# Optimization experiments

Hardware: AMD Instinct MI355X
Metric: run time of the kernel (lower is better)

## Reference

```python
import jax, jax.numpy as jnp
import numpy as np

WS = 7          # window size (7x7)
N = WS * WS     # tokens per window = 49
C = 192         # channels
H = 6           # heads
NW = 64         # windows per image (for mask)
B_ = 8192       # num_windows * batch


def _rel_index():
    coords = np.stack(np.meshgrid(np.arange(WS), np.arange(WS), indexing='ij'))  # [2,7,7]
    cf = coords.reshape(2, -1)                       # [2,49]
    rc = (cf[:, :, None] - cf[:, None, :]).transpose(1, 2, 0).astype(np.int64)  # [49,49,2]
    rc[..., 0] += WS - 1
    rc[..., 1] += WS - 1
    rc[..., 0] *= 2 * WS - 1
    return jnp.asarray(rc.sum(-1), dtype=jnp.int32)  # [49,49], values in [0, 169)


def setup_inputs() -> dict:
    key = jax.random.key(0)
    ks = jax.random.split(key, 10)
    std = 0.02
    return {
        'xq': jax.random.normal(ks[0], (B_, N, C), dtype=jnp.float32),
        'mask': jax.random.normal(ks[1], (NW, N, N), dtype=jnp.float32),
        'Wq': jax.random.normal(ks[2], (C, C), dtype=jnp.float32) * std,
        'bq': jnp.zeros((C,), dtype=jnp.float32),
        'Wkv': jax.random.normal(ks[3], (C, 2 * C), dtype=jnp.float32) * std,
        'bkv': jnp.zeros((2 * C,), dtype=jnp.float32),
        'Wproj': jax.random.normal(ks[4], (C, C), dtype=jnp.float32) * std,
        'bproj': jnp.zeros((C,), dtype=jnp.float32),
        'bias_table': jax.random.normal(ks[5], ((2 * WS - 1) * (2 * WS - 1), H), dtype=jnp.float32) * std,
        'rel_index': _rel_index(),
    }


def reference(xq, mask, Wq, bq, Wkv, bkv, Wproj, bproj, bias_table, rel_index):
    b_, n, c = xq.shape
    h = H
    dh = c // h
    scale = dh ** (-0.5)
    # projections (xkv = xq since xkv is None in the original call)
    q = (xq @ Wq + bq).reshape(b_, n, h, dh).transpose(0, 2, 1, 3) * scale      # [b_,h,n,dh]
    kv = (xq @ Wkv + bkv).reshape(b_, n, 2, h, dh).transpose(2, 0, 3, 1, 4)     # [2,b_,h,n,dh]
    k, v = kv[0], kv[1]
    attn = jnp.einsum('bhqd,bhkd->bhqk', q, k)                                   # [b_,h,n,n]
    # gathered relative-position bias: [n,n,h] -> [h,n,n]
    bias = bias_table[rel_index.reshape(-1)].reshape(n, n, h).transpose(2, 0, 1)
    attn = attn + bias[None]
    # mask add: [b_//nw, nw, h, n, n] + [1, nw, 1, n, n]
    nw = mask.shape[0]
    attn = attn.reshape(b_ // nw, nw, h, n, n) + mask[None, :, None]
    attn = jax.nn.softmax(attn.reshape(b_, h, n, n), axis=-1)
    x = jnp.einsum('bhqk,bhkd->bhqd', attn, v).transpose(0, 2, 1, 3).reshape(b_, n, c)
    return x @ Wproj + bproj
```

## Files before the change

kernel.cpp:

```cpp
#include <hip/hip_runtime.h>


#define NTOK 49
#define NPAD 64
#define CCH 192
#define NHEAD 6
#define DH 32

typedef __bf16 bf16_t;
typedef bf16_t bf16x8 __attribute__((ext_vector_type(8)));
typedef bf16_t bf16x4 __attribute__((ext_vector_type(4)));
typedef float f32x4 __attribute__((ext_vector_type(4)));

#define WS_WQT   0
#define WS_WKVT  73728
#define WS_WPT   221184
#define WS_BIASG 294912

__global__ void prep_kernel(const float* __restrict__ Wq, const float* __restrict__ Wkv,
                            const float* __restrict__ Wproj, const float* __restrict__ btab,
                            const int* __restrict__ rel,
                            bf16_t* __restrict__ wqt, bf16_t* __restrict__ wkvt,
                            bf16_t* __restrict__ wpt, float* __restrict__ biasg) {
    int i = blockIdx.x * 256 + threadIdx.x;
    if (i < 36864) { int n = i / 192, k = i % 192; wqt[i] = (bf16_t)Wq[k * 192 + n]; }
    int j = i - 36864;
    if (j >= 0 && j < 73728) { int n = j / 192, k = j % 192; wkvt[j] = (bf16_t)Wkv[k * 384 + n]; }
    int p = i - 110592;
    if (p >= 0 && p < 36864) { int n = p / 192, k = p % 192; wpt[p] = (bf16_t)Wproj[k * 192 + n]; }
    int q = i - 147456;
    if (q >= 0 && q < 14406) { int h = q / 2401, rc = q % 2401; biasg[q] = btab[rel[rc] * 6 + h]; }
}

__global__ __launch_bounds__(512) void wattn_kernel(
    const float* __restrict__ xq, const float* __restrict__ mask,
    const float* __restrict__ bq, const float* __restrict__ bkv, const float* __restrict__ bproj,
    const bf16_t* __restrict__ wqt, const bf16_t* __restrict__ wkvt, const bf16_t* __restrict__ wpt,
    const float* __restrict__ biasg, float* __restrict__ out)
{
    __shared__ __align__(16) unsigned char smem[114688];
    unsigned char* Xs = smem;
    unsigned char* Qs = smem + 24576;
    unsigned char* Ks = smem + 49152;
    unsigned char* Vt = smem + 73728;
    unsigned char* Ps = smem + 98304;

    const int tid = threadIdx.x;
    const int wid = tid >> 6;
    const int lane = tid & 63;
    const int l15 = lane & 15;
    const int lg = lane >> 4;
    const int b = blockIdx.x;
    const float* xp = xq + (size_t)b * (NTOK * CCH);

    for (int idx = tid; idx < 2352; idx += 512) {
        int row = idx / 48;
        int cb = (idx % 48) * 4;
        float4 v = *(const float4*)(xp + row * 192 + cb);
        bf16x4 pk = { (bf16_t)v.x, (bf16_t)v.y, (bf16_t)v.z, (bf16_t)v.w };
        *(bf16x4*)(Xs + row * 384 + ((cb * 2) ^ ((row & 7) << 4))) = pk;
    }
    for (int idx = tid; idx < 720; idx += 512) {
        *(unsigned long long*)(Xs + 49 * 384 + idx * 8) = 0ULL;
    }
    __syncthreads();

    const float SCALE = 0.17677669529663687f;
    for (int nt = wid; nt < 36; nt += 8) {
        int m = nt / 12;
        int ncol = (nt % 12) * 16;
        const bf16_t* WT; const float* bias;
        if (m == 0)      { WT = wqt  + (size_t)ncol * 192;        bias = bq + ncol; }
        else if (m == 1) { WT = wkvt + (size_t)ncol * 192;        bias = bkv + ncol; }
        else             { WT = wkvt + (size_t)(192 + ncol) * 192; bias = bkv + 192 + ncol; }
        bf16x8 bfr[6];
        const bf16_t* wrow = WT + (size_t)l15 * 192 + lg * 8;
#pragma unroll
        for (int ks = 0; ks < 6; ks++) bfr[ks] = *(const bf16x8*)(wrow + ks * 32);
        float bv = bias[l15];
#pragma unroll
        for (int mt = 0; mt < 4; mt++) {
            f32x4 acc = { bv, bv, bv, bv };
#pragma unroll
            for (int ks = 0; ks < 6; ks++) {
                int row = mt * 16 + l15;
                int cb = ks * 32 + lg * 8;
                bf16x8 a = *(const bf16x8*)(Xs + row * 384 + ((cb * 2) ^ ((row & 7) << 4)));
                acc = __builtin_amdgcn_mfma_f32_16x16x32_bf16(a, bfr[ks], acc, 0, 0, 0);
            }
            if (m == 0) {
#pragma unroll
                for (int j = 0; j < 4; j++) acc[j] *= SCALE;
            }
#pragma unroll
            for (int j = 0; j < 4; j++) {
                int col = ncol + l15;
                if (m == 2) {
                    int rr = col;
                    int tc = mt * 16 + lg * 4 + j;
                    *(bf16_t*)(Vt + rr * 128 + ((tc * 2) ^ ((rr & 7) << 4))) = (bf16_t)acc[j];
                } else {
                    int rr = mt * 16 + lg * 4 + j;
                    unsigned char* dst = (m == 0) ? Qs : Ks;
                    *(bf16_t*)(dst + rr * 384 + ((col * 2) ^ ((rr & 7) << 4))) = (bf16_t)acc[j];
                }
            }
        }
    }
    __syncthreads();

    const int widx = b & 63;
    const float* maskw = mask + (size_t)widx * 2401;
    unsigned char* Pw = Ps + wid * 2048;

    for (int k3 = 0; k3 < 3; k3++) {
        int u = wid + 8 * k3;
        int h = u >> 2, qt = u & 3;
        int qrow = qt * 16 + l15;
        int qcb = h * 32 + lg * 8;
        bf16x8 afr = *(const bf16x8*)(Qs + qrow * 384 + ((qcb * 2) ^ ((qrow & 7) << 4)));
        f32x4 s[4];
#pragma unroll
        for (int f = 0; f < 4; f++) {
            int krow = f * 16 + l15;
            bf16x8 kfr = *(const bf16x8*)(Ks + krow * 384 + ((qcb * 2) ^ ((krow & 7) << 4)));
            f32x4 z = { 0.f, 0.f, 0.f, 0.f };
            s[f] = __builtin_amdgcn_mfma_f32_16x16x32_bf16(afr, kfr, z, 0, 0, 0);
        }
        const float* bgh = biasg + h * 2401;
#pragma unroll
        for (int f = 0; f < 4; f++) {
            int c = f * 16 + l15;
#pragma unroll
            for (int j = 0; j < 4; j++) {
                int r = qt * 16 + lg * 4 + j;
                if (c >= 49) s[f][j] = -1e30f;
                else if (r < 49) s[f][j] += bgh[r * 49 + c] + maskw[r * 49 + c];
            }
        }
        float mx[4], rs[4];
#pragma unroll
        for (int j = 0; j < 4; j++) {
            float m0 = fmaxf(fmaxf(s[0][j], s[1][j]), fmaxf(s[2][j], s[3][j]));
#pragma unroll
            for (int d = 1; d < 16; d <<= 1) m0 = fmaxf(m0, __shfl_xor(m0, d, 16));
            mx[j] = m0;
        }
#pragma unroll
        for (int j = 0; j < 4; j++) {
            float t = 0.f;
#pragma unroll
            for (int f = 0; f < 4; f++) { s[f][j] = __expf(s[f][j] - mx[j]); t += s[f][j]; }
#pragma unroll
            for (int d = 1; d < 16; d <<= 1) t += __shfl_xor(t, d, 16);
            rs[j] = 1.0f / t;
        }
#pragma unroll
        for (int f = 0; f < 4; f++) {
            int c = f * 16 + l15;
#pragma unroll
            for (int j = 0; j < 4; j++) {
                int rr = lg * 4 + j;
                *(bf16_t*)(Pw + rr * 128 + ((c * 2) ^ ((rr & 7) << 4))) = (bf16_t)(s[f][j] * rs[j]);
            }
        }
        __threadfence_block();
        bf16x8 pa[2];
#pragma unroll
        for (int ks = 0; ks < 2; ks++) {
            int pcb = ks * 32 + lg * 8;
            pa[ks] = *(const bf16x8*)(Pw + l15 * 128 + ((pcb * 2) ^ ((l15 & 7) << 4)));
        }
#pragma unroll
        for (int dt = 0; dt < 2; dt++) {
            f32x4 acc = { 0.f, 0.f, 0.f, 0.f };
#pragma unroll
            for (int ks = 0; ks < 2; ks++) {
                int vr = h * 32 + dt * 16 + l15;
                int vcb = ks * 32 + lg * 8;
                bf16x8 vfr = *(const bf16x8*)(Vt + vr * 128 + ((vcb * 2) ^ ((vr & 7) << 4)));
                acc = __builtin_amdgcn_mfma_f32_16x16x32_bf16(pa[ks], vfr, acc, 0, 0, 0);
            }
#pragma unroll
            for (int j = 0; j < 4; j++) {
                int orow = qt * 16 + lg * 4 + j;
                int ocol = h * 32 + dt * 16 + l15;
                *(bf16_t*)(Xs + orow * 384 + ((ocol * 2) ^ ((orow & 7) << 4))) = (bf16_t)acc[j];
            }
        }
    }
    __syncthreads();

    float* op = out + (size_t)b * (NTOK * CCH);
    for (int nt = wid; nt < 12; nt += 8) {
        int ncol = nt * 16;
        bf16x8 bfr[6];
        const bf16_t* wrow = wpt + (size_t)(ncol + l15) * 192 + lg * 8;
#pragma unroll
        for (int ks = 0; ks < 6; ks++) bfr[ks] = *(const bf16x8*)(wrow + ks * 32);
        float bv = bproj[ncol + l15];
#pragma unroll
        for (int mt = 0; mt < 4; mt++) {
            f32x4 acc = { bv, bv, bv, bv };
#pragma unroll
            for (int ks = 0; ks < 6; ks++) {
                int row = mt * 16 + l15;
                int cb = ks * 32 + lg * 8;
                bf16x8 a = *(const bf16x8*)(Xs + row * 384 + ((cb * 2) ^ ((row & 7) << 4)));
                acc = __builtin_amdgcn_mfma_f32_16x16x32_bf16(a, bfr[ks], acc, 0, 0, 0);
            }
#pragma unroll
            for (int j = 0; j < 4; j++) {
                int r = mt * 16 + lg * 4 + j;
                if (r < 49) op[r * 192 + ncol + l15] = acc[j];
            }
        }
    }
}

extern "C" void kernel_launch(void* const* d_in, const int* in_sizes, int n_in,
                              void* d_out, int out_size, void* d_ws, size_t ws_size,
                              hipStream_t stream) {
    const float* xq    = (const float*)d_in[0];
    const float* mask  = (const float*)d_in[1];
    const float* Wq    = (const float*)d_in[2];
    const float* bq    = (const float*)d_in[3];
    const float* Wkv   = (const float*)d_in[4];
    const float* bkv   = (const float*)d_in[5];
    const float* Wproj = (const float*)d_in[6];
    const float* bproj = (const float*)d_in[7];
    const float* btab  = (const float*)d_in[8];
    const int*   rel   = (const int*)d_in[9];
    float* out = (float*)d_out;

    char* ws = (char*)d_ws;
    bf16_t* wqt   = (bf16_t*)(ws + WS_WQT);
    bf16_t* wkvt  = (bf16_t*)(ws + WS_WKVT);
    bf16_t* wpt   = (bf16_t*)(ws + WS_WPT);
    float*  biasg = (float*)(ws + WS_BIASG);

    prep_kernel<<<633, 256, 0, stream>>>(Wq, Wkv, Wproj, btab, rel, wqt, wkvt, wpt, biasg);
    wattn_kernel<<<8192, 512, 0, stream>>>(xq, mask, bq, bkv, bproj, wqt, wkvt, wpt, biasg, out);
}
```

Baseline: 733.7 us.

## Double block to 1024 threads, precombine bias+mask table, vectorize MFMA stores

Launches 16 waves per window instead of 8 and rebalances the QKV, attention and output-projection work evenly across them. The attention scale is folded into Wq and bq in the prep kernel, and relative bias plus mask is precombined into a padded table so each lane reads float4 values. Operand order of the MFMAs is swapped so results come out transposed, which allows packed bf16x4 and float4 stores and a two-shuffle softmax reduction. The costs are a larger prep kernel that writes about 4MB, a larger LDS footprint, and higher register pressure at 1024 threads.

```diff
diff --git a/kernel.cpp b/kernel.cpp
--- a/kernel.cpp
+++ b/kernel.cpp
@@ -2,10 +2,7 @@
 
 
 #define NTOK 49
-#define NPAD 64
 #define CCH 192
-#define NHEAD 6
-#define DH 32
 
 typedef __bf16 bf16_t;
 typedef bf16_t bf16x8 __attribute__((ext_vector_type(8)));
@@ -15,35 +12,57 @@
 #define WS_WQT   0
 #define WS_WKVT  73728
 #define WS_WPT   221184
-#define WS_BIASG 294912
-
-__global__ void prep_kernel(const float* __restrict__ Wq, const float* __restrict__ Wkv,
-                            const float* __restrict__ Wproj, const float* __restrict__ btab,
-                            const int* __restrict__ rel,
+#define WS_BQS   294912
+#define WS_TBL   295680
+
+#define SWZ(row, off) ((off) ^ (((row) & 7) << 4))
+
+__global__ void prep_kernel(const float* __restrict__ Wq, const float* __restrict__ bq,
+                            const float* __restrict__ Wkv, const float* __restrict__ Wproj,
+                            const float* __restrict__ btab, const int* __restrict__ rel,
+                            const float* __restrict__ mask,
                             bf16_t* __restrict__ wqt, bf16_t* __restrict__ wkvt,
-                            bf16_t* __restrict__ wpt, float* __restrict__ biasg) {
-    int i = blockIdx.x * 256 + threadIdx.x;
-    if (i < 36864) { int n = i / 192, k = i % 192; wqt[i] = (bf16_t)Wq[k * 192 + n]; }
-    int j = i - 36864;
-    if (j >= 0 && j < 73728) { int n = j / 192, k = j % 192; wkvt[j] = (bf16_t)Wkv[k * 384 + n]; }
-    int p = i - 110592;
-    if (p >= 0 && p < 36864) { int n = p / 192, k = p % 192; wpt[p] = (bf16_t)Wproj[k * 192 + n]; }
-    int q = i - 147456;
-    if (q >= 0 && q < 14406) { int h = q / 2401, rc = q % 2401; biasg[q] = btab[rel[rc] * 6 + h]; }
+                            bf16_t* __restrict__ wpt, float* __restrict__ bqs,
+                            float* __restrict__ tbl, int mode) {
+    const float SC = 0.17677669529663687f;
+    long i = (long)blockIdx.x * 256 + threadIdx.x;
+    if (i < 36864) { int n = i / 192, k = i % 192; wqt[i] = (bf16_t)(Wq[k * 192 + n] * SC); return; }
+    i -= 36864;
+    if (i < 73728) { int n = i / 192, k = i % 192; wkvt[i] = (bf16_t)Wkv[k * 384 + n]; return; }
+    i -= 73728;
+    if (i < 36864) { int n = i / 192, k = i % 192; wpt[i] = (bf16_t)Wproj[k * 192 + n]; return; }
+    i -= 36864;
+    if (i < 192) { bqs[i] = bq[i] * SC; return; }
+    i -= 192;
+    if (mode == 0) {
+        if (i < 979072) {
+            int c = i % 52; long r = i / 52; int q = r % 49; r /= 49; int h = r % 6; int w = r / 6;
+            tbl[i] = (c < 49) ? (btab[rel[q * 49 + c] * 6 + h] + mask[(size_t)w * 2401 + q * 49 + c]) : 0.f;
+        }
+    } else if (mode == 1) {
+        if (i < 15288) { int c = i % 52; int r = i / 52; int q = r % 49; int h = r / 49;
+            tbl[i] = (c < 49) ? btab[rel[q * 49 + c] * 6 + h] : 0.f; return; }
+        i -= 15288;
+        if (i < 163072) { int c = i % 52; long r = i / 52; int q = r % 49; int w = r / 49;
+            tbl[15288 + i] = (c < 49) ? mask[(size_t)w * 2401 + q * 49 + c] : 0.f; }
+    } else {
+        if (i < 14406) { int h = i / 2401, rc = i % 2401; tbl[i] = btab[rel[rc] * 6 + h]; }
+    }
 }
 
-__global__ __launch_bounds__(512) void wattn_kernel(
+__global__ __launch_bounds__(1024, 4) void wattn_kernel(
     const float* __restrict__ xq, const float* __restrict__ mask,
-    const float* __restrict__ bq, const float* __restrict__ bkv, const float* __restrict__ bproj,
+    const float* __restrict__ bkv, const float* __restrict__ bproj,
     const bf16_t* __restrict__ wqt, const bf16_t* __restrict__ wkvt, const bf16_t* __restrict__ wpt,
-    const float* __restrict__ biasg, float* __restrict__ out)
+    const float* __restrict__ bqs, const float* __restrict__ tbl,
+    float* __restrict__ out, int mode)
 {
-    __shared__ __align__(16) unsigned char smem[114688];
-    unsigned char* Xs = smem;
-    unsigned char* Qs = smem + 24576;
-    unsigned char* Ks = smem + 49152;
-    unsigned char* Vt = smem + 73728;
-    unsigned char* Ps = smem + 98304;
+    __shared__ __align__(16) unsigned char smem[131072];
+    unsigned char* XsO = smem;
+    unsigned char* Qs  = smem + 24576;
+    unsigned char* Ks  = smem + 49152;
+    unsigned char* Vt  = smem + 73728;
+    unsigned char* Ps  = smem + 98304;
 
     const int tid = threadIdx.x;
     const int wid = tid >> 6;
@@ -53,166 +72,176 @@
     const int b = blockIdx.x;
     const float* xp = xq + (size_t)b * (NTOK * CCH);
 
-    for (int idx = tid; idx < 2352; idx += 512) {
+    for (int idx = tid; idx < 2352; idx += 1024) {
         int row = idx / 48;
-        int cb = (idx % 48) * 4;
-        float4 v = *(const float4*)(xp + row * 192 + cb);
+        int c4 = idx % 48;
+        float4 v = *(const float4*)(xp + row * 192 + c4 * 4);
         bf16x4 pk = { (bf16_t)v.x, (bf16_t)v.y, (bf16_t)v.z, (bf16_t)v.w };
-        *(bf16x4*)(Xs + row * 384 + ((cb * 2) ^ ((row & 7) << 4))) = pk;
-    }
-    for (int idx = tid; idx < 720; idx += 512) {
-        *(unsigned long long*)(Xs + 49 * 384 + idx * 8) = 0ULL;
-    }
+        *(bf16x4*)(XsO + row * 384 + SWZ(row, c4 * 8)) = pk;
+    }
+    if (tid < 720) *(unsigned long long*)(XsO + 49 * 384 + tid * 8) = 0ULL;
     __syncthreads();
 
-    const float SCALE = 0.17677669529663687f;
-    for (int nt = wid; nt < 36; nt += 8) {
-        int m = nt / 12;
-        int ncol = (nt % 12) * 16;
-        const bf16_t* WT; const float* bias;
-        if (m == 0)      { WT = wqt  + (size_t)ncol * 192;        bias = bq + ncol; }
-        else if (m == 1) { WT = wkvt + (size_t)ncol * 192;        bias = bkv + ncol; }
-        else             { WT = wkvt + (size_t)(192 + ncol) * 192; bias = bkv + 192 + ncol; }
+    {
         bf16x8 bfr[6];
-        const bf16_t* wrow = WT + (size_t)l15 * 192 + lg * 8;
-#pragma unroll
-        for (int ks = 0; ks < 6; ks++) bfr[ks] = *(const bf16x8*)(wrow + ks * 32);
-        float bv = bias[l15];
-#pragma unroll
-        for (int mt = 0; mt < 4; mt++) {
-            f32x4 acc = { bv, bv, bv, bv };
-#pragma unroll
-            for (int ks = 0; ks < 6; ks++) {
-                int row = mt * 16 + l15;
-                int cb = ks * 32 + lg * 8;
-                bf16x8 a = *(const bf16x8*)(Xs + row * 384 + ((cb * 2) ^ ((row & 7) << 4)));
-                acc = __builtin_amdgcn_mfma_f32_16x16x32_bf16(a, bfr[ks], acc, 0, 0, 0);
-            }
-            if (m == 0) {
-#pragma unroll
-                for (int j = 0; j < 4; j++) acc[j] *= SCALE;
+        float4 bias4;
+        float bv = 0.f;
+        int prev_ut = -1;
+        for (int u = 9 * wid; u < 9 * wid + 9; ++u) {
+            int ut = u >> 2, mt = u & 3;
+            bool isV = (ut >= 24);
+            if (ut != prev_ut) {
+                prev_ut = ut;
+                const bf16_t* wrow;
+                if (ut < 12)      wrow = wqt  + (size_t)(ut * 16 + l15) * 192;
+                else if (ut < 24) wrow = wkvt + (size_t)((ut - 12) * 16 + l15) * 192;
+                else              wrow = wkvt + (size_t)(192 + (ut - 24) * 16 + l15) * 192;
+#pragma unroll
+                for (int ks = 0; ks < 6; ks++) bfr[ks] = *(const bf16x8*)(wrow + ks * 32 + lg * 8);
+                if (!isV) {
+                    const float* bp = (ut < 12) ? (bqs + ut * 16) : (bkv + (ut - 12) * 16);
+                    bias4 = *(const float4*)(bp + lg * 4);
+                } else {
+                    bv = bkv[192 + (ut - 24) * 16 + l15];
+                }
+            }
+            int xrow = mt * 16 + l15;
+            bf16x8 xf[6];
+#pragma unroll
+            for (int ks = 0; ks < 6; ks++)
+                xf[ks] = *(const bf16x8*)(XsO + xrow * 384 + SWZ(xrow, ks * 64 + lg * 16));
+            if (!isV) {
+                f32x4 acc = { bias4.x, bias4.y, bias4.z, bias4.w };
+#pragma unroll
+                for (int ks = 0; ks < 6; ks++)
+                    acc = __builtin_amdgcn_mfma_f32_16x16x32_bf16(bfr[ks], xf[ks], acc, 0, 0, 0);
+                int ncol = (ut < 12 ? ut : ut - 12) * 16;
+                unsigned char* dst = (ut < 12) ? Qs : Ks;
+                bf16x4 pk = { (bf16_t)acc[0], (bf16_t)acc[1], (bf16_t)acc[2], (bf16_t)acc[3] };
+                int trow = mt * 16 + l15;
+                *(bf16x4*)(dst + trow * 384 + SWZ(trow, ncol * 2 + lg * 8)) = pk;
+            } else {
+                f32x4 acc = { bv, bv, bv, bv };
+#pragma unroll
+                for (int ks = 0; ks < 6; ks++)
+                    acc = __builtin_amdgcn_mfma_f32_16x16x32_bf16(xf[ks], bfr[ks], acc, 0, 0, 0);
+                int crow = (ut - 24) * 16 + l15;
+                bf16x4 pk = { (bf16_t)acc[0], (bf16_t)acc[1], (bf16_t)acc[2], (bf16_t)acc[3] };
+                *(bf16x4*)(Vt + crow * 128 + SWZ(crow, mt * 32 + lg * 8)) = pk;
+            }
+        }
+    }
+    __syncthreads();
+
+    const int widx = b & 63;
+    unsigned char* Pw = Ps + wid * 2048;
+    for (int u = wid; u < 24; u += 16) {
+        int h = u >> 2, qt = u & 3;
+        int cb = h * 64 + lg * 16;
+        int qrow = qt * 16 + l15;
+        bf16x8 qfr = *(const bf16x8*)(Qs + qrow * 384 + SWZ(qrow, cb));
+        f32x4 s[4];
+#pragma unroll
+        for (int f = 0; f < 4; f++) {
+            int kr = f * 16 + l15;
+            bf16x8 kfr = *(const bf16x8*)(Ks + kr * 384 + SWZ(kr, cb));
+            f32x4 z = { 0.f, 0.f, 0.f, 0.f };
+            s[f] = __builtin_amdgcn_mfma_f32_16x16x32_bf16(kfr, qfr, z, 0, 0, 0);
+        }
+        int q = qt * 16 + l15;
+        bool qok = (q < 49);
+#pragma unroll
+        for (int f = 0; f < 4; f++) {
+            int kb = f * 16 + lg * 4;
+            float4 a = { 0.f, 0.f, 0.f, 0.f };
+            if (qok && kb < 49) {
+                if (mode == 0) {
+                    a = *(const float4*)(tbl + (((size_t)(widx * 6 + h) * 49 + q) * 52 + kb));
+                } else if (mode == 1) {
+                    float4 b1 = *(const float4*)(tbl + ((size_t)(h * 49 + q) * 52 + kb));
+                    float4 m1 = *(const float4*)(tbl + 15288 + (((size_t)widx * 49 + q) * 52 + kb));
+                    a.x = b1.x + m1.x; a.y = b1.y + m1.y; a.z = b1.z + m1.z; a.w = b1.w + m1.w;
+                }
             }
 #pragma unroll
             for (int j = 0; j < 4; j++) {
-                int col = ncol + l15;
-                if (m == 2) {
-                    int rr = col;
-                    int tc = mt * 16 + lg * 4 + j;
-                    *(bf16_t*)(Vt + rr * 128 + ((tc * 2) ^ ((rr & 7) << 4))) = (bf16_t)acc[j];
-                } else {
-                    int rr = mt * 16 + lg * 4 + j;
-                    unsigned char* dst = (m == 0) ? Qs : Ks;
-                    *(bf16_t*)(dst + rr * 384 + ((col * 2) ^ ((rr & 7) << 4))) = (bf16_t)acc[j];
+                int k = kb + j;
+                float av = (j == 0) ? a.x : (j == 1) ? a.y : (j == 2) ? a.z : a.w;
+                if (mode == 2) {
+                    av = 0.f;
+                    if (qok && k < 49)
+                        av = tbl[h * 2401 + q * 49 + k] + mask[(size_t)widx * 2401 + q * 49 + k];
                 }
-            }
-        }
-    }
-    __syncthreads();
-
-    const int widx = b & 63;
-    const float* maskw = mask + (size_t)widx * 2401;
-    unsigned char* Pw = Ps + wid * 2048;
-
-    for (int k3 = 0; k3 < 3; k3++) {
-        int u = wid + 8 * k3;
-        int h = u >> 2, qt = u & 3;
-        int qrow = qt * 16 + l15;
-        int qcb = h * 32 + lg * 8;
-        bf16x8 afr = *(const bf16x8*)(Qs + qrow * 384 + ((qcb * 2) ^ ((qrow & 7) << 4)));
-        f32x4 s[4];
+                if (k >= 49) s[f][j] = -1e30f;
+                else if (qok) s[f][j] += av;
+            }
+        }
+        float m = -1e30f;
+#pragma unroll
+        for (int f = 0; f < 4; f++)
+#pragma unroll
+            for (int j = 0; j < 4; j++) m = fmaxf(m, s[f][j]);
+        m = fmaxf(m, __shfl_xor(m, 16));
+        m = fmaxf(m, __shfl_xor(m, 32));
+        float t = 0.f;
+#pragma unroll
+        for (int f = 0; f < 4; f++)
+#pragma unroll
+            for (int j = 0; j < 4; j++) { s[f][j] = __expf(s[f][j] - m); t += s[f][j]; }
+        t += __shfl_xor(t, 16);
+        t += __shfl_xor(t, 32);
+        float inv = 1.0f / t;
 #pragma unroll
         for (int f = 0; f < 4; f++) {
-            int krow = f * 16 + l15;
-            bf16x8 kfr = *(const bf16x8*)(Ks + krow * 384 + ((qcb * 2) ^ ((krow & 7) << 4)));
-            f32x4 z = { 0.f, 0.f, 0.f, 0.f };
-            s[f] = __builtin_amdgcn_mfma_f32_16x16x32_bf16(afr, kfr, z, 0, 0, 0);
-        }
-        const float* bgh = biasg + h * 2401;
-#pragma unroll
-        for (int f = 0; f < 4; f++) {
-            int c = f * 16 + l15;
-#pragma unroll
-            for (int j = 0; j < 4; j++) {
-                int r = qt * 16 + lg * 4 + j;
-                if (c >= 49) s[f][j] = -1e30f;
-                else if (r < 49) s[f][j] += bgh[r * 49 + c] + maskw[r * 49 + c];
-            }
-        }
-        float mx[4], rs[4];
-#pragma unroll
-        for (int j = 0; j < 4; j++) {
-            float m0 = fmaxf(fmaxf(s[0][j], s[1][j]), fmaxf(s[2][j], s[3][j]));
-#pragma unroll
-            for (int d = 1; d < 16; d <<= 1) m0 = fmaxf(m0, __shfl_xor(m0, d, 16));
-            mx[j] = m0;
-        }
-#pragma unroll
-        for (int j = 0; j < 4; j++) {
-            float t = 0.f;
-#pragma unroll
-            for (int f = 0; f < 4; f++) { s[f][j] = __expf(s[f][j] - mx[j]); t += s[f][j]; }
-#pragma unroll
-            for (int d = 1; d < 16; d <<= 1) t += __shfl_xor(t, d, 16);
-            rs[j] = 1.0f / t;
-        }
-#pragma unroll
-        for (int f = 0; f < 4; f++) {
-            int c = f * 16 + l15;
-#pragma unroll
-            for (int j = 0; j < 4; j++) {
-                int rr = lg * 4 + j;
-                *(bf16_t*)(Pw + rr * 128 + ((c * 2) ^ ((rr & 7) << 4))) = (bf16_t)(s[f][j] * rs[j]);
-            }
+            bf16x4 pk = { (bf16_t)(s[f][0] * inv), (bf16_t)(s[f][1] * inv),
+                          (bf16_t)(s[f][2] * inv), (bf16_t)(s[f][3] * inv) };
+            *(bf16x4*)(Pw + l15 * 128 + SWZ(l15, f * 32 + lg * 8)) = pk;
         }
         __threadfence_block();
         bf16x8 pa[2];
 #pragma unroll
-        for (int ks = 0; ks < 2; ks++) {
-            int pcb = ks * 32 + lg * 8;
-            pa[ks] = *(const bf16x8*)(Pw + l15 * 128 + ((pcb * 2) ^ ((l15 & 7) << 4)));
-        }
+        for (int ks = 0; ks < 2; ks++)
+            pa[ks] = *(const bf16x8*)(Pw + l15 * 128 + SWZ(l15, ks * 64 + lg * 16));
 #pragma unroll
         for (int dt = 0; dt < 2; dt++) {
             f32x4 acc = { 0.f, 0.f, 0.f, 0.f };
 #pragma unroll
             for (int ks = 0; ks < 2; ks++) {
                 int vr = h * 32 + dt * 16 + l15;
-                int vcb = ks * 32 + lg * 8;
-                bf16x8 vfr = *(const bf16x8*)(Vt + vr * 128 + ((vcb * 2) ^ ((vr & 7) << 4)));
-                acc = __builtin_amdgcn_mfma_f32_16x16x32_bf16(pa[ks], vfr, acc, 0, 0, 0);
-            }
-#pragma unroll
-            for (int j = 0; j < 4; j++) {
-                int orow = qt * 16 + lg * 4 + j;
-                int ocol = h * 32 + dt * 16 + l15;
-                *(bf16_t*)(Xs + orow * 384 + ((ocol * 2) ^ ((orow & 7) << 4))) = (bf16_t)acc[j];
-            }
+                bf16x8 vfr = *(const bf16x8*)(Vt + vr * 128 + SWZ(vr, ks * 64 + lg * 16));
+                acc = __builtin_amdgcn_mfma_f32_16x16x32_bf16(vfr, pa[ks], acc, 0, 0, 0);
+            }
+            int orow = qt * 16 + l15;
+            bf16x4 pk = { (bf16_t)acc[0], (bf16_t)acc[1], (bf16_t)acc[2], (bf16_t)acc[3] };
+            *(bf16x4*)(XsO + orow * 384 + SWZ(orow, h * 64 + dt * 32 + lg * 8)) = pk;
         }
     }
     __syncthreads();
 
-    float* op = out + (size_t)b * (NTOK * CCH);
-    for (int nt = wid; nt < 12; nt += 8) {
-        int ncol = nt * 16;
+    {
+        float* op = out + (size_t)b * (NTOK * CCH);
         bf16x8 bfr[6];
-        const bf16_t* wrow = wpt + (size_t)(ncol + l15) * 192 + lg * 8;
-#pragma unroll
-        for (int ks = 0; ks < 6; ks++) bfr[ks] = *(const bf16x8*)(wrow + ks * 32);
-        float bv = bproj[ncol + l15];
-#pragma unroll
-        for (int mt = 0; mt < 4; mt++) {
-            f32x4 acc = { bv, bv, bv, bv };
+        float4 bias4 = { 0.f, 0.f, 0.f, 0.f };
+        int prev_nt = -1;
+        for (int u = 3 * wid; u < 3 * wid + 3; ++u) {
+            int nt = u >> 2, mt = u & 3;
+            if (nt != prev_nt) {
+                prev_nt = nt;
+                const bf16_t* wrow = wpt + (size_t)(nt * 16 + l15) * 192;
+#pragma unroll
+                for (int ks = 0; ks < 6; ks++) bfr[ks] = *(const bf16x8*)(wrow + ks * 32 + lg * 8);
+                bias4 = *(const float4*)(bproj + nt * 16 + lg * 4);
+            }
+            int orow = mt * 16 + l15;
+            f32x4 acc = { bias4.x, bias4.y, bias4.z, bias4.w };
 #pragma unroll
             for (int ks = 0; ks < 6; ks++) {
-                int row = mt * 16 + l15;
-                int cb = ks * 32 + lg * 8;
-                bf16x8 a = *(const bf16x8*)(Xs + row * 384 + ((cb * 2) ^ ((row & 7) << 4)));
-                acc = __builtin_amdgcn_mfma_f32_16x16x32_bf16(a, bfr[ks], acc, 0, 0, 0);
-            }
-#pragma unroll
-            for (int j = 0; j < 4; j++) {
-                int r = mt * 16 + lg * 4 + j;
-                if (r < 49) op[r * 192 + ncol + l15] = acc[j];
+                bf16x8 of = *(const bf16x8*)(XsO + orow * 384 + SWZ(orow, ks * 64 + lg * 16));
+                acc = __builtin_amdgcn_mfma_f32_16x16x32_bf16(bfr[ks], of, acc, 0, 0, 0);
+            }
+            if (orow < 49) {
+                float4 st = { acc[0], acc[1], acc[2], acc[3] };
+                *(float4*)(op + orow * 192 + nt * 16 + lg * 4) = st;
             }
         }
     }
@@ -234,11 +263,20 @@
     float* out = (float*)d_out;
 
     char* ws = (char*)d_ws;
-    bf16_t* wqt   = (bf16_t*)(ws + WS_WQT);
-    bf16_t* wkvt  = (bf16_t*)(ws + WS_WKVT);
-    bf16_t* wpt   = (bf16_t*)(ws + WS_WPT);
-    float*  biasg = (float*)(ws + WS_BIASG);
-
-    prep_kernel<<<633, 256, 0, stream>>>(Wq, Wkv, Wproj, btab, rel, wqt, wkvt, wpt, biasg);
-    wattn_kernel<<<8192, 512, 0, stream>>>(xq, mask, bq, bkv, bproj, wqt, wkvt, wpt, biasg, out);
+    bf16_t* wqt  = (bf16_t*)(ws + WS_WQT);
+    bf16_t* wkvt = (bf16_t*)(ws + WS_WKVT);
+    bf16_t* wpt  = (bf16_t*)(ws + WS_WPT);
+    float*  bqs  = (float*)(ws + WS_BQS);
+    float*  tbl  = (float*)(ws + WS_TBL);
+
+    size_t need0 = (size_t)WS_TBL + 979072u * 4u;
+    size_t need1 = (size_t)WS_TBL + 178360u * 4u;
+    int mode = (ws_size >= need0) ? 0 : (ws_size >= need1 ? 1 : 2);
+
+    long prep_elems = 147648L + (mode == 0 ? 979072L : (mode == 1 ? 178360L : 14406L));
+    int prep_blocks = (int)((prep_elems + 255) / 256);
+    prep_kernel<<<prep_blocks, 256, 0, stream>>>(Wq, bq, Wkv, Wproj, btab, rel, mask,
+                                                 wqt, wkvt, wpt, bqs, tbl, mode);
+    wattn_kernel<<<8192, 1024, 0, stream>>>(xq, mask, bkv, bproj, wqt, wkvt, wpt,
+                                            bqs, tbl, out, mode);
 }
```

Result: faster. 642.4 us (-12.4%).
